# Kernel tuning notes

Measured on AMD Instinct MI355X. Metric: run time of the kernel, lower is better.

## Reference

```python
import jax, jax.numpy as jnp
import numpy as np

N, C, IMG, HEADS = 512, 3, 32, 4
F = C * IMG * IMG          # 3072 node feature dim
E = 4096                   # edges without self loops
EPS = 1e-5                 # BatchNorm eps
SLOPE = 0.2                # GATv2 LeakyReLU negative slope


def bn(x, g, b, m, v):
    # eval-mode BatchNorm2d over channel dim 1
    inv = g / jnp.sqrt(v + EPS)
    return x * inv[None, :, None, None] + (b - m * inv)[None, :, None, None]


def conv1x1(x, W, b):
    # W: [out_c, in_c]
    return jnp.einsum('bchw,oc->bohw', x, W) + b[None, :, None, None]


def setup_inputs():
    key = jax.random.key(0)
    ks = jax.random.split(key, 32)
    inp = {}
    inp['x'] = jax.random.normal(ks[0], (N, C, IMG, IMG), jnp.float32)
    src = jax.random.randint(ks[1], (E,), 0, N)
    off = jax.random.randint(ks[2], (E,), 1, N)
    inp['edge_index'] = jnp.stack([src, (src + off) % N]).astype(jnp.int32)  # no self loops

    def w(k, shape, fan_in):
        return jax.random.normal(k, shape, jnp.float32) / np.sqrt(fan_in)

    i = 3
    def nk():
        nonlocal i; i += 1; return ks[i - 1]
    # grapher fc1: Conv2d(C,C,1)+BN
    inp['fc1_W'] = w(nk(), (C, C), C); inp['fc1_b'] = jnp.zeros((C,), jnp.float32)
    inp['bn1_g'] = jnp.ones((C,), jnp.float32); inp['bn1_b'] = jnp.zeros((C,), jnp.float32)
    inp['bn1_m'] = 0.1 * jax.random.normal(nk(), (C,), jnp.float32)
    inp['bn1_v'] = jax.random.uniform(nk(), (C,), jnp.float32, 0.5, 1.5)
    # GATv2Conv(F, F, heads=HEADS): lin_l, lin_r [F, HEADS*F] with bias, att [HEADS, F], out bias
    inp['Wl'] = w(nk(), (F, HEADS * F), F); inp['bl'] = jnp.zeros((HEADS * F,), jnp.float32)
    inp['Wr'] = w(nk(), (F, HEADS * F), F); inp['br'] = jnp.zeros((HEADS * F,), jnp.float32)
    inp['att'] = w(nk(), (HEADS, F), F)
    inp['gat_b'] = jnp.zeros((HEADS * F,), jnp.float32)
    # grapher fc2: Conv2d(C*HEADS, C, 1)+BN
    inp['fc2_W'] = w(nk(), (C, C * HEADS), C * HEADS); inp['fc2_b'] = jnp.zeros((C,), jnp.float32)
    inp['bn2_g'] = jnp.ones((C,), jnp.float32); inp['bn2_b'] = jnp.zeros((C,), jnp.float32)
    inp['bn2_m'] = 0.1 * jax.random.normal(nk(), (C,), jnp.float32)
    inp['bn2_v'] = jax.random.uniform(nk(), (C,), jnp.float32, 0.5, 1.5)
    # FFN fc1 / fc2 (C->C 1x1 conv + BN)
    inp['ffn1_W'] = w(nk(), (C, C), C); inp['ffn1_b'] = jnp.zeros((C,), jnp.float32)
    inp['bnf1_g'] = jnp.ones((C,), jnp.float32); inp['bnf1_b'] = jnp.zeros((C,), jnp.float32)
    inp['bnf1_m'] = 0.1 * jax.random.normal(nk(), (C,), jnp.float32)
    inp['bnf1_v'] = jax.random.uniform(nk(), (C,), jnp.float32, 0.5, 1.5)
    inp['ffn2_W'] = w(nk(), (C, C), C); inp['ffn2_b'] = jnp.zeros((C,), jnp.float32)
    inp['bnf2_g'] = jnp.ones((C,), jnp.float32); inp['bnf2_b'] = jnp.zeros((C,), jnp.float32)
    inp['bnf2_m'] = 0.1 * jax.random.normal(nk(), (C,), jnp.float32)
    inp['bnf2_v'] = jax.random.uniform(nk(), (C,), jnp.float32, 0.5, 1.5)
    return inp


def reference(x, edge_index, fc1_W, fc1_b, bn1_g, bn1_b, bn1_m, bn1_v,
              Wl, bl, Wr, br, att, gat_b,
              fc2_W, fc2_b, bn2_g, bn2_b, bn2_m, bn2_v,
              ffn1_W, ffn1_b, bnf1_g, bnf1_b, bnf1_m, bnf1_v,
              ffn2_W, ffn2_b, bnf2_g, bnf2_b, bnf2_m, bnf2_v):
    shortcut = x
    h = bn(conv1x1(x, fc1_W, fc1_b), bn1_g, bn1_b, bn1_m, bn1_v)
    hf = h.reshape(N, F)
    xl = (hf @ Wl + bl).reshape(N, HEADS, F)  # source transform
    xr = (hf @ Wr + br).reshape(N, HEADS, F)  # target transform
    # add self loops (PyG GATv2Conv default)
    loops = jnp.arange(N, dtype=edge_index.dtype)
    src = jnp.concatenate([edge_index[0], loops])
    dst = jnp.concatenate([edge_index[1], loops])
    # GATv2 edge scores: a . LeakyReLU(xl_j + xr_i)
    e = jax.nn.leaky_relu(xl[src] + xr[dst], negative_slope=SLOPE)  # [E+N, HEADS, F]
    logits = jnp.einsum('ehf,hf->eh', e, att)
    mx = jax.ops.segment_max(logits, dst, num_segments=N)
    ex = jnp.exp(logits - jax.lax.stop_gradient(mx)[dst])
    denom = jax.ops.segment_sum(ex, dst, num_segments=N)
    alpha = ex / denom[dst]                                          # segment softmax over targets
    agg = jax.ops.segment_sum(xl[src] * alpha[:, :, None], dst, num_segments=N)  # [N, HEADS, F]
    g_out = (agg.reshape(N, HEADS * F) + gat_b).reshape(N, C * HEADS, IMG, IMG)
    g = bn(conv1x1(g_out, fc2_W, fc2_b), bn2_g, bn2_b, bn2_m, bn2_v) + shortcut
    # FFN with residual
    f = jax.nn.relu(bn(conv1x1(g, ffn1_W, ffn1_b), bnf1_g, bnf1_b, bnf1_m, bnf1_v))
    f = bn(conv1x1(f, ffn2_W, ffn2_b), bnf2_g, bnf2_b, bnf2_m, bnf2_v)
    return f + g
```

## Files before the change

### kernel.cpp

```cpp
#include <hip/hip_runtime.h>

#define N_NODES 512
#define FDIM    3072
#define HEADS   4
#define HFD     12288
#define E_IN    4096
#define E_TOT   4608
#define EPSV    1e-5f
#define SLOPE   0.2f
#define LCAP    256

typedef unsigned short u16;
typedef unsigned int   u32;

typedef short s16x8 __attribute__((ext_vector_type(8)));
typedef float f32x4 __attribute__((ext_vector_type(4)));

__device__ __forceinline__ u16 f2bf(float f){
  u32 u = __builtin_bit_cast(u32, f);
  u = (u + 0x7fffu + ((u >> 16) & 1u)) >> 16;
  return (u16)u;
}
__device__ __forceinline__ float bf2f(u16 h){
  return __builtin_bit_cast(float, ((u32)h) << 16);
}
__device__ __forceinline__ float bflo(u32 p){
  return __builtin_bit_cast(float, p << 16);
}
__device__ __forceinline__ float bfhi(u32 p){
  return __builtin_bit_cast(float, p & 0xffff0000u);
}

__device__ __forceinline__ void gl_lds16(const u16* g, u16* l){
  __builtin_amdgcn_global_load_lds(
      (const __attribute__((address_space(1))) unsigned int*)g,
      (__attribute__((address_space(3))) unsigned int*)l, 16, 0, 0);
}

__global__ void k_csr(const int* __restrict__ ei, int* __restrict__ cnt,
                      int* __restrict__ off, int* __restrict__ elist){
  __shared__ int s[512];
  __shared__ int cur[512];
  int t = threadIdx.x;
  s[t] = 0;
  __syncthreads();
  for (int e = t; e < E_TOT; e += 512){
    int d = (e < E_IN) ? ei[E_IN + e] : (e - E_IN);
    atomicAdd(&s[d], 1);
  }
  __syncthreads();
  int v = s[t];
  cnt[t] = v;
  for (int dd = 1; dd < 512; dd <<= 1){
    int add = (t >= dd) ? s[t - dd] : 0;
    __syncthreads();
    s[t] += add;
    __syncthreads();
  }
  int exc = s[t] - v;
  off[t] = exc;
  cur[t] = exc;
  __syncthreads();
  for (int e = t; e < E_TOT; e += 512){
    int d = (e < E_IN) ? ei[E_IN + e] : (e - E_IN);
    int pos = atomicAdd(&cur[d], 1);
    elist[pos] = e;
  }
}

__global__ void k_fc1(const float* __restrict__ x, const float* __restrict__ W,
                      const float* __restrict__ b, const float* __restrict__ g,
                      const float* __restrict__ bb, const float* __restrict__ m,
                      const float* __restrict__ v, u16* __restrict__ hf){
  int id = blockIdx.x * 256 + threadIdx.x;
  int n = id >> 10, p = id & 1023;
  float x0 = x[n * FDIM + p];
  float x1 = x[n * FDIM + 1024 + p];
  float x2 = x[n * FDIM + 2048 + p];
#pragma unroll
  for (int c = 0; c < 3; ++c){
    float t = b[c] + W[c*3+0]*x0 + W[c*3+1]*x1 + W[c*3+2]*x2;
    float inv = g[c] * rsqrtf(v[c] + EPSV);
    float o = t * inv + (bb[c] - m[c] * inv);
    hf[n * FDIM + c * 1024 + p] = f2bf(o);
  }
}

__global__ __launch_bounds__(256, 3) void k_gemm(
    const u16* __restrict__ hf, const float* __restrict__ Wl,
    const float* __restrict__ bl, const float* __restrict__ Wr,
    const float* __restrict__ br, u16* __restrict__ xl, u16* __restrict__ xr){
  __shared__ u16 As[2][256 * 32];
  __shared__ u16 Bs[2][64 * 40];

  const int tid  = threadIdx.x;
  const int wave = tid >> 6, lane = tid & 63;
  const int quad = lane >> 4, l16 = lane & 15;

  const int g = blockIdx.x;
  const int ntile = (g >> 4) * 8 + (g & 7);
  const int mhalf = (g >> 3) & 1;
  const int n0 = ntile * 64;
  const int rbase = mhalf * 256;

  const float* Wg; const float* biasp; u16* outp; int cb;
  if (n0 < HFD){ Wg = Wl; biasp = bl; outp = xl; cb = n0; }
  else         { Wg = Wr; biasp = br; outp = xr; cb = n0 - HFD; }

  const u16* ga = hf + (size_t)(rbase + wave * 64 + (lane >> 2)) * FDIM
                     + (((lane & 3) ^ ((lane >> 3) & 3)) << 3);

  const int bn = tid & 63, bkh = tid >> 6;
  const float* gb = Wg + (size_t)bkh * 8 * HFD + (cb + bn);
  const int bwo = bn * 40 + bkh * 8;

  const int araw = (wave * 64 + l16) * 32 + ((quad ^ ((l16 >> 1) & 3)) << 3);
  const int brd  = l16 * 40 + quad * 8;

  f32x4 acc[4][4];
#pragma unroll
  for (int i = 0; i < 4; ++i)
#pragma unroll
    for (int j = 0; j < 4; ++j) acc[i][j] = (f32x4){0.f, 0.f, 0.f, 0.f};

  float bv[8];
#pragma unroll
  for (int j = 0; j < 8; ++j) bv[j] = gb[(size_t)j * HFD];
#pragma unroll
  for (int i = 0; i < 4; ++i)
    gl_lds16(ga + (size_t)i * 16 * FDIM, As[0] + (wave * 4 + i) * 512);
  {
    u32 p0 = (u32)f2bf(bv[0]) | ((u32)f2bf(bv[1]) << 16);
    u32 p1 = (u32)f2bf(bv[2]) | ((u32)f2bf(bv[3]) << 16);
    u32 p2 = (u32)f2bf(bv[4]) | ((u32)f2bf(bv[5]) << 16);
    u32 p3 = (u32)f2bf(bv[6]) | ((u32)f2bf(bv[7]) << 16);
    *(uint4*)(Bs[0] + bwo) = make_uint4(p0, p1, p2, p3);
  }
#pragma unroll
  for (int j = 0; j < 8; ++j) bv[j] = gb[(size_t)(32 + j) * HFD];
  __syncthreads();

#define GEMM_BODY(KS, CUR, NXT)                                               \
  {                                                                           \
    const int ksv = (KS);                                                     \
    if (ksv < 95){                                                            \
      _Pragma("unroll")                                                       \
      for (int i = 0; i < 4; ++i)                                             \
        gl_lds16(ga + (size_t)i * 16 * FDIM + (ksv + 1) * 32,                 \
                 As[NXT] + (wave * 4 + i) * 512);                             \
      u32 p0 = (u32)f2bf(bv[0]) | ((u32)f2bf(bv[1]) << 16);                   \
      u32 p1 = (u32)f2bf(bv[2]) | ((u32)f2bf(bv[3]) << 16);                   \
      u32 p2 = (u32)f2bf(bv[4]) | ((u32)f2bf(bv[5]) << 16);                   \
      u32 p3 = (u32)f2bf(bv[6]) | ((u32)f2bf(bv[7]) << 16);                   \
      *(uint4*)(Bs[NXT] + bwo) = make_uint4(p0, p1, p2, p3);                  \
      int kn = (ksv + 2 < 96 ? ksv + 2 : 95) * 32;                            \
      _Pragma("unroll")                                                       \
      for (int j = 0; j < 8; ++j) bv[j] = gb[(size_t)(kn + j) * HFD];         \
    }                                                                         \
    s16x8 af[4], bfr[4];                                                      \
    _Pragma("unroll")                                                         \
    for (int i = 0; i < 4; ++i)                                               \
      af[i] = __builtin_bit_cast(s16x8, *(const uint4*)(As[CUR] + araw + i * 512)); \
    _Pragma("unroll")                                                         \
    for (int j = 0; j < 4; ++j)                                               \
      bfr[j] = __builtin_bit_cast(s16x8, *(const uint4*)(Bs[CUR] + brd + j * 640)); \
    _Pragma("unroll")                                                         \
    for (int i = 0; i < 4; ++i)                                               \
      _Pragma("unroll")                                                       \
      for (int j = 0; j < 4; ++j)                                             \
        acc[i][j] = __builtin_amdgcn_mfma_f32_16x16x32_bf16(af[i], bfr[j], acc[i][j], 0, 0, 0); \
    __syncthreads();                                                          \
  }

  for (int ks = 0; ks < 96; ks += 2){
    GEMM_BODY(ks, 0, 1);
    GEMM_BODY(ks + 1, 1, 0);
  }
#undef GEMM_BODY

  float bj[4];
#pragma unroll
  for (int j = 0; j < 4; ++j) bj[j] = biasp[cb + j * 16 + l16];
#pragma unroll
  for (int i = 0; i < 4; ++i){
    int mrow = rbase + wave * 64 + i * 16 + quad * 4;
#pragma unroll
    for (int r = 0; r < 4; ++r){
      u16* orow = outp + (size_t)(mrow + r) * HFD + cb + l16;
#pragma unroll
      for (int j = 0; j < 4; ++j)
        orow[j * 16] = f2bf(acc[i][j][r] + bj[j]);
    }
  }
}

__global__ __launch_bounds__(256) void k_lsm(
    const int* __restrict__ ei, const int* __restrict__ cnt,
    const int* __restrict__ off, const int* __restrict__ elist,
    const u16* __restrict__ xl, const u16* __restrict__ xr,
    const float* __restrict__ att, float* __restrict__ alpha){
  __shared__ float s_log[LCAP][5];
  __shared__ int   s_e[LCAP];
  const int n = blockIdx.x;
  const int t = threadIdx.x;
  const int h = t >> 6, lane = t & 63;
  const int deg = cnt[n], st = off[n];
  const int f0 = lane * 48;

  float xrf[48], av[48];
  {
    const u16* xrp = xr + (size_t)n * HFD + h * FDIM + f0;
    const float* ap = att + h * FDIM + f0;
#pragma unroll
    for (int k = 0; k < 6; ++k){
      uint4 a = *(const uint4*)(xrp + k * 8);
      xrf[k*8+0]=bflo(a.x); xrf[k*8+1]=bfhi(a.x);
      xrf[k*8+2]=bflo(a.y); xrf[k*8+3]=bfhi(a.y);
      xrf[k*8+4]=bflo(a.z); xrf[k*8+5]=bfhi(a.z);
      xrf[k*8+6]=bflo(a.w); xrf[k*8+7]=bfhi(a.w);
      float4 w0 = *(const float4*)(ap + k * 8);
      float4 w1 = *(const float4*)(ap + k * 8 + 4);
      av[k*8+0]=w0.x; av[k*8+1]=w0.y; av[k*8+2]=w0.z; av[k*8+3]=w0.w;
      av[k*8+4]=w1.x; av[k*8+5]=w1.y; av[k*8+6]=w1.z; av[k*8+7]=w1.w;
    }
  }

  auto edge_logit = [&](int s_node) -> float {
    const u16* xlp = xl + (size_t)s_node * HFD + h * FDIM + f0;
    float acc = 0.f;
#pragma unroll
    for (int k = 0; k < 6; ++k){
      uint4 a = *(const uint4*)(xlp + k * 8);
      float z;
      z = bflo(a.x) + xrf[k*8+0]; z = z > 0.f ? z : SLOPE * z; acc += z * av[k*8+0];
      z = bfhi(a.x) + xrf[k*8+1]; z = z > 0.f ? z : SLOPE * z; acc += z * av[k*8+1];
      z = bflo(a.y) + xrf[k*8+2]; z = z > 0.f ? z : SLOPE * z; acc += z * av[k*8+2];
      z = bfhi(a.y) + xrf[k*8+3]; z = z > 0.f ? z : SLOPE * z; acc += z * av[k*8+3];
      z = bflo(a.z) + xrf[k*8+4]; z = z > 0.f ? z : SLOPE * z; acc += z * av[k*8+4];
      z = bfhi(a.z) + xrf[k*8+5]; z = z > 0.f ? z : SLOPE * z; acc += z * av[k*8+5];
      z = bflo(a.w) + xrf[k*8+6]; z = z > 0.f ? z : SLOPE * z; acc += z * av[k*8+6];
      z = bfhi(a.w) + xrf[k*8+7]; z = z > 0.f ? z : SLOPE * z; acc += z * av[k*8+7];
    }
#pragma unroll
    for (int o = 32; o > 0; o >>= 1) acc += __shfl_down(acc, o);
    return acc;
  };

  if (deg <= LCAP){
    for (int jb = 0; jb < deg; ++jb){
      int e = elist[st + jb];
      if (t == 0) s_e[jb] = e;
      int s = (e < E_IN) ? ei[e] : (e - E_IN);
      float lg = edge_logit(s);
      if (lane == 0) s_log[jb][h] = lg;
    }
    __syncthreads();
    float mx = -1e30f;
    for (int j = lane; j < deg; j += 64) mx = fmaxf(mx, s_log[j][h]);
#pragma unroll
    for (int o = 32; o > 0; o >>= 1) mx = fmaxf(mx, __shfl_down(mx, o));
    mx = __shfl(mx, 0);
    float sm = 0.f;
    for (int j = lane; j < deg; j += 64) sm += __expf(s_log[j][h] - mx);
#pragma unroll
    for (int o = 32; o > 0; o >>= 1) sm += __shfl_down(sm, o);
    sm = __shfl(sm, 0);
    float rs = 1.f / sm;
    for (int j = lane; j < deg; j += 64)
      alpha[s_e[j] * 4 + h] = __expf(s_log[j][h] - mx) * rs;
  } else {
    for (int jb = 0; jb < deg; ++jb){
      int e = elist[st + jb];
      int s = (e < E_IN) ? ei[e] : (e - E_IN);
      float lg = edge_logit(s);
      if (lane == 0) alpha[e * 4 + h] = lg;
    }
    float mx = -1e30f;
    for (int j = lane; j < deg; j += 64){
      int e = elist[st + j];
      mx = fmaxf(mx, alpha[e * 4 + h]);
    }
#pragma unroll
    for (int o = 32; o > 0; o >>= 1) mx = fmaxf(mx, __shfl_down(mx, o));
    mx = __shfl(mx, 0);
    float sm = 0.f;
    for (int j = lane; j < deg; j += 64){
      int e = elist[st + j];
      sm += __expf(alpha[e * 4 + h] - mx);
    }
#pragma unroll
    for (int o = 32; o > 0; o >>= 1) sm += __shfl_down(sm, o);
    sm = __shfl(sm, 0);
    float rs = 1.f / sm;
    for (int j = lane; j < deg; j += 64){
      int e = elist[st + j];
      alpha[e * 4 + h] = __expf(alpha[e * 4 + h] - mx) * rs;
    }
  }
}

__global__ __launch_bounds__(256) void k_aggfinal(
    const int* __restrict__ ei, const int* __restrict__ cnt,
    const int* __restrict__ off, const int* __restrict__ elist,
    const float* __restrict__ alpha, const u16* __restrict__ xl,
    const float* __restrict__ gat_b,
    const float* __restrict__ W2, const float* __restrict__ b2,
    const float* __restrict__ g2, const float* __restrict__ bb2,
    const float* __restrict__ m2, const float* __restrict__ v2,
    const float* __restrict__ W3, const float* __restrict__ b3,
    const float* __restrict__ g3, const float* __restrict__ bb3,
    const float* __restrict__ m3, const float* __restrict__ v3,
    const float* __restrict__ W4, const float* __restrict__ b4,
    const float* __restrict__ g4, const float* __restrict__ bb4,
    const float* __restrict__ m4, const float* __restrict__ v4,
    const float* __restrict__ x, float* __restrict__ out){
  __shared__ int    s_src[128];
  __shared__ float4 s_al[128];
  const int n = blockIdx.x;
  const int t = threadIdx.x;
  const int p4 = t * 4;
  const int deg = cnt[n], st = off[n];

  float acc[12][4];
#pragma unroll
  for (int o = 0; o < 12; ++o)
#pragma unroll
    for (int r = 0; r < 4; ++r) acc[o][r] = 0.f;

  for (int base = 0; base < deg; base += 128){
    int cn = min(deg - base, 128);
    if (t < cn){
      int e = elist[st + base + t];
      s_src[t] = (e < E_IN) ? ei[e] : (e - E_IN);
      s_al[t] = *(const float4*)(alpha + e * 4);
    }
    __syncthreads();
    for (int j = 0; j < cn; ++j){
      int s = s_src[j];
      float4 al4 = s_al[j];
      float alh[4] = {al4.x, al4.y, al4.z, al4.w};
      const u16* bp = xl + (size_t)s * HFD;
#pragma unroll
      for (int h = 0; h < 4; ++h){
#pragma unroll
        for (int c = 0; c < 3; ++c){
          ushort4 xv = *(const ushort4*)(bp + h * FDIM + c * 1024 + p4);
          acc[h*3+c][0] += alh[h] * bf2f(xv.x);
          acc[h*3+c][1] += alh[h] * bf2f(xv.y);
          acc[h*3+c][2] += alh[h] * bf2f(xv.z);
          acc[h*3+c][3] += alh[h] * bf2f(xv.w);
        }
      }
    }
    __syncthreads();
  }

#pragma unroll
  for (int o = 0; o < 12; ++o){
    float4 gv = *(const float4*)(gat_b + o * 1024 + p4);
    acc[o][0] += gv.x; acc[o][1] += gv.y; acc[o][2] += gv.z; acc[o][3] += gv.w;
  }
  float xv[3][4];
#pragma unroll
  for (int c = 0; c < 3; ++c){
    float4 t4 = *(const float4*)(x + (size_t)n * FDIM + c * 1024 + p4);
    xv[c][0] = t4.x; xv[c][1] = t4.y; xv[c][2] = t4.z; xv[c][3] = t4.w;
  }
  float o4[3][4];
#pragma unroll
  for (int r = 0; r < 4; ++r){
    float gch[3];
#pragma unroll
    for (int c = 0; c < 3; ++c){
      float tt = b2[c];
#pragma unroll
      for (int o = 0; o < 12; ++o) tt += W2[c * 12 + o] * acc[o][r];
      float inv = g2[c] * rsqrtf(v2[c] + EPSV);
      gch[c] = tt * inv + (bb2[c] - m2[c] * inv) + xv[c][r];
    }
    float f1[3];
#pragma unroll
    for (int c = 0; c < 3; ++c){
      float tt = b3[c] + W3[c*3+0]*gch[0] + W3[c*3+1]*gch[1] + W3[c*3+2]*gch[2];
      float inv = g3[c] * rsqrtf(v3[c] + EPSV);
      float vv = tt * inv + (bb3[c] - m3[c] * inv);
      f1[c] = fmaxf(vv, 0.f);
    }
#pragma unroll
    for (int c = 0; c < 3; ++c){
      float tt = b4[c] + W4[c*3+0]*f1[0] + W4[c*3+1]*f1[1] + W4[c*3+2]*f1[2];
      float inv = g4[c] * rsqrtf(v4[c] + EPSV);
      o4[c][r] = tt * inv + (bb4[c] - m4[c] * inv) + gch[c];
    }
  }
#pragma unroll
  for (int c = 0; c < 3; ++c)
    *(float4*)(out + (size_t)n * FDIM + c * 1024 + p4) =
        make_float4(o4[c][0], o4[c][1], o4[c][2], o4[c][3]);
}

extern "C" void kernel_launch(void* const* d_in, const int* in_sizes, int n_in,
                              void* d_out, int out_size, void* d_ws, size_t ws_size,
                              hipStream_t stream){
  (void)in_sizes; (void)n_in; (void)out_size; (void)ws_size;
  const float* x     = (const float*)d_in[0];
  const int*   ei    = (const int*)d_in[1];
  const float* fc1_W = (const float*)d_in[2];
  const float* fc1_b = (const float*)d_in[3];
  const float* bn1_g = (const float*)d_in[4];
  const float* bn1_b = (const float*)d_in[5];
  const float* bn1_m = (const float*)d_in[6];
  const float* bn1_v = (const float*)d_in[7];
  const float* Wl    = (const float*)d_in[8];
  const float* bl    = (const float*)d_in[9];
  const float* Wr    = (const float*)d_in[10];
  const float* br    = (const float*)d_in[11];
  const float* att   = (const float*)d_in[12];
  const float* gat_b = (const float*)d_in[13];
  const float* fc2_W = (const float*)d_in[14];
  const float* fc2_b = (const float*)d_in[15];
  const float* bn2_g = (const float*)d_in[16];
  const float* bn2_b = (const float*)d_in[17];
  const float* bn2_m = (const float*)d_in[18];
  const float* bn2_v = (const float*)d_in[19];
  const float* ffn1_W= (const float*)d_in[20];
  const float* ffn1_b= (const float*)d_in[21];
  const float* bnf1_g= (const float*)d_in[22];
  const float* bnf1_b= (const float*)d_in[23];
  const float* bnf1_m= (const float*)d_in[24];
  const float* bnf1_v= (const float*)d_in[25];
  const float* ffn2_W= (const float*)d_in[26];
  const float* ffn2_b= (const float*)d_in[27];
  const float* bnf2_g= (const float*)d_in[28];
  const float* bnf2_b= (const float*)d_in[29];
  const float* bnf2_m= (const float*)d_in[30];
  const float* bnf2_v= (const float*)d_in[31];

  char* w = (char*)d_ws;
  u16*   hf     = (u16*)(w);
  u16*   xl     = (u16*)(w + 3145728);
  u16*   xr     = (u16*)(w + 15728640);
  float* alpha  = (float*)(w + 28385280);
  int*   cnt    = (int*)(w + 28459008);
  int*   offp   = (int*)(w + 28461056);
  int*   elist  = (int*)(w + 28465152);

  k_csr<<<1, 512, 0, stream>>>(ei, cnt, offp, elist);
  k_fc1<<<2048, 256, 0, stream>>>(x, fc1_W, fc1_b, bn1_g, bn1_b, bn1_m, bn1_v, hf);
  k_gemm<<<768, 256, 0, stream>>>(hf, Wl, bl, Wr, br, xl, xr);
  k_lsm<<<512, 256, 0, stream>>>(ei, cnt, offp, elist, xl, xr, att, alpha);
  k_aggfinal<<<512, 256, 0, stream>>>(ei, cnt, offp, elist, alpha, xl, gat_b,
                                      fc2_W, fc2_b, bn2_g, bn2_b, bn2_m, bn2_v,
                                      ffn1_W, ffn1_b, bnf1_g, bnf1_b, bnf1_m, bnf1_v,
                                      ffn2_W, ffn2_b, bnf2_g, bnf2_b, bnf2_m, bnf2_v,
                                      x, (float*)d_out);
}
```

Baseline: 525.1 us.

## Fuse CSR build into fc1 kernel and fuse softmax with aggregation

```diff
diff --git a/kernel.cpp b/kernel.cpp
--- a/kernel.cpp
+++ b/kernel.cpp
@@ -8,7 +8,7 @@
 #define E_TOT   4608
 #define EPSV    1e-5f
 #define SLOPE   0.2f
-#define LCAP    256
+#define LCAP    128
 
 typedef unsigned short u16;
 typedef unsigned int   u32;
@@ -37,52 +37,54 @@
       (__attribute__((address_space(3))) unsigned int*)l, 16, 0, 0);
 }
 
-__global__ void k_csr(const int* __restrict__ ei, int* __restrict__ cnt,
-                      int* __restrict__ off, int* __restrict__ elist){
-  __shared__ int s[512];
-  __shared__ int cur[512];
-  int t = threadIdx.x;
-  s[t] = 0;
-  __syncthreads();
-  for (int e = t; e < E_TOT; e += 512){
-    int d = (e < E_IN) ? ei[E_IN + e] : (e - E_IN);
-    atomicAdd(&s[d], 1);
-  }
-  __syncthreads();
-  int v = s[t];
-  cnt[t] = v;
-  for (int dd = 1; dd < 512; dd <<= 1){
-    int add = (t >= dd) ? s[t - dd] : 0;
-    __syncthreads();
-    s[t] += add;
-    __syncthreads();
-  }
-  int exc = s[t] - v;
-  off[t] = exc;
-  cur[t] = exc;
-  __syncthreads();
-  for (int e = t; e < E_TOT; e += 512){
-    int d = (e < E_IN) ? ei[E_IN + e] : (e - E_IN);
-    int pos = atomicAdd(&cur[d], 1);
-    elist[pos] = e;
-  }
-}
-
-__global__ void k_fc1(const float* __restrict__ x, const float* __restrict__ W,
-                      const float* __restrict__ b, const float* __restrict__ g,
-                      const float* __restrict__ bb, const float* __restrict__ m,
-                      const float* __restrict__ v, u16* __restrict__ hf){
-  int id = blockIdx.x * 256 + threadIdx.x;
-  int n = id >> 10, p = id & 1023;
-  float x0 = x[n * FDIM + p];
-  float x1 = x[n * FDIM + 1024 + p];
-  float x2 = x[n * FDIM + 2048 + p];
-#pragma unroll
-  for (int c = 0; c < 3; ++c){
-    float t = b[c] + W[c*3+0]*x0 + W[c*3+1]*x1 + W[c*3+2]*x2;
-    float inv = g[c] * rsqrtf(v[c] + EPSV);
-    float o = t * inv + (bb[c] - m[c] * inv);
-    hf[n * FDIM + c * 1024 + p] = f2bf(o);
+__global__ __launch_bounds__(256) void k_pre(
+    const float* __restrict__ x, const float* __restrict__ W,
+    const float* __restrict__ b, const float* __restrict__ g,
+    const float* __restrict__ bb, const float* __restrict__ m,
+    const float* __restrict__ v, u16* __restrict__ hf,
+    const int* __restrict__ ei, int* __restrict__ cnt,
+    int* __restrict__ off, int* __restrict__ elist){
+  if (blockIdx.x < 2048){
+    int id = blockIdx.x * 256 + threadIdx.x;
+    int n = id >> 10, p = id & 1023;
+    float x0 = x[n * FDIM + p];
+    float x1 = x[n * FDIM + 1024 + p];
+    float x2 = x[n * FDIM + 2048 + p];
+#pragma unroll
+    for (int c = 0; c < 3; ++c){
+      float t = b[c] + W[c*3+0]*x0 + W[c*3+1]*x1 + W[c*3+2]*x2;
+      float inv = g[c] * rsqrtf(v[c] + EPSV);
+      float o = t * inv + (bb[c] - m[c] * inv);
+      hf[n * FDIM + c * 1024 + p] = f2bf(o);
+    }
+  } else {
+    __shared__ int sa[512], sb[512];
+    int t = threadIdx.x;
+    sa[t] = 0; sa[t + 256] = 0;
+    __syncthreads();
+    for (int e = t; e < E_TOT; e += 256){
+      int d = (e < E_IN) ? ei[E_IN + e] : (e - E_IN);
+      atomicAdd(&sa[d], 1);
+    }
+    __syncthreads();
+    int c0 = sa[t], c1 = sa[t + 256];
+    cnt[t] = c0; cnt[t + 256] = c1;
+    int* src = sa; int* dst = sb;
+    for (int d = 1; d < 512; d <<= 1){
+      dst[t] = src[t] + (t >= d ? src[t - d] : 0);
+      int i2 = t + 256;
+      dst[i2] = src[i2] + (i2 >= d ? src[i2 - d] : 0);
+      __syncthreads();
+      int* tmp = src; src = dst; dst = tmp;
+    }
+    off[t] = src[t] - c0; off[t + 256] = src[t + 256] - c1;
+    dst[t] = src[t] - c0; dst[t + 256] = src[t + 256] - c1;
+    __syncthreads();
+    for (int e = t; e < E_TOT; e += 256){
+      int d = (e < E_IN) ? ei[E_IN + e] : (e - E_IN);
+      int pos = atomicAdd(&dst[d], 1);
+      elist[pos] = e;
+    }
   }
 }
 
@@ -194,13 +196,25 @@
   }
 }
 
-__global__ __launch_bounds__(256) void k_lsm(
+__global__ __launch_bounds__(256) void k_post(
     const int* __restrict__ ei, const int* __restrict__ cnt,
     const int* __restrict__ off, const int* __restrict__ elist,
     const u16* __restrict__ xl, const u16* __restrict__ xr,
-    const float* __restrict__ att, float* __restrict__ alpha){
+    const float* __restrict__ att, float* __restrict__ alpha,
+    const float* __restrict__ gat_b,
+    const float* __restrict__ W2, const float* __restrict__ b2,
+    const float* __restrict__ g2, const float* __restrict__ bb2,
+    const float* __restrict__ m2, const float* __restrict__ v2,
+    const float* __restrict__ W3, const float* __restrict__ b3,
+    const float* __restrict__ g3, const float* __restrict__ bb3,
+    const float* __restrict__ m3, const float* __restrict__ v3,
+    const float* __restrict__ W4, const float* __restrict__ b4,
+    const float* __restrict__ g4, const float* __restrict__ bb4,
+    const float* __restrict__ m4, const float* __restrict__ v4,
+    const float* __restrict__ x, float* __restrict__ out){
   __shared__ float s_log[LCAP][5];
-  __shared__ int   s_e[LCAP];
+  __shared__ __align__(16) float s_alf[LCAP][4];
+  __shared__ int s_src[LCAP];
   const int n = blockIdx.x;
   const int t = threadIdx.x;
   const int h = t >> 6, lane = t & 63;
@@ -246,11 +260,12 @@
     return acc;
   };
 
-  if (deg <= LCAP){
+  const bool small = (deg <= LCAP);
+  if (small){
     for (int jb = 0; jb < deg; ++jb){
       int e = elist[st + jb];
-      if (t == 0) s_e[jb] = e;
       int s = (e < E_IN) ? ei[e] : (e - E_IN);
+      if (t == 0) s_src[jb] = s;
       float lg = edge_logit(s);
       if (lane == 0) s_log[jb][h] = lg;
     }
@@ -267,7 +282,8 @@
     sm = __shfl(sm, 0);
     float rs = 1.f / sm;
     for (int j = lane; j < deg; j += 64)
-      alpha[s_e[j] * 4 + h] = __expf(s_log[j][h] - mx) * rs;
+      s_alf[j][h] = __expf(s_log[j][h] - mx) * rs;
+    __syncthreads();
   } else {
     for (int jb = 0; jb < deg; ++jb){
       int e = elist[st + jb];
@@ -275,6 +291,7 @@
       float lg = edge_logit(s);
       if (lane == 0) alpha[e * 4 + h] = lg;
     }
+    __syncthreads();
     float mx = -1e30f;
     for (int j = lane; j < deg; j += 64){
       int e = elist[st + j];
@@ -296,63 +313,60 @@
       int e = elist[st + j];
       alpha[e * 4 + h] = __expf(alpha[e * 4 + h] - mx) * rs;
     }
-  }
-}
-
-__global__ __launch_bounds__(256) void k_aggfinal(
-    const int* __restrict__ ei, const int* __restrict__ cnt,
-    const int* __restrict__ off, const int* __restrict__ elist,
-    const float* __restrict__ alpha, const u16* __restrict__ xl,
-    const float* __restrict__ gat_b,
-    const float* __restrict__ W2, const float* __restrict__ b2,
-    const float* __restrict__ g2, const float* __restrict__ bb2,
-    const float* __restrict__ m2, const float* __restrict__ v2,
-    const float* __restrict__ W3, const float* __restrict__ b3,
-    const float* __restrict__ g3, const float* __restrict__ bb3,
-    const float* __restrict__ m3, const float* __restrict__ v3,
-    const float* __restrict__ W4, const float* __restrict__ b4,
-    const float* __restrict__ g4, const float* __restrict__ bb4,
-    const float* __restrict__ m4, const float* __restrict__ v4,
-    const float* __restrict__ x, float* __restrict__ out){
-  __shared__ int    s_src[128];
-  __shared__ float4 s_al[128];
-  const int n = blockIdx.x;
-  const int t = threadIdx.x;
+    __syncthreads();
+  }
+
   const int p4 = t * 4;
-  const int deg = cnt[n], st = off[n];
-
   float acc[12][4];
 #pragma unroll
   for (int o = 0; o < 12; ++o)
 #pragma unroll
     for (int r = 0; r < 4; ++r) acc[o][r] = 0.f;
 
-  for (int base = 0; base < deg; base += 128){
-    int cn = min(deg - base, 128);
-    if (t < cn){
-      int e = elist[st + base + t];
-      s_src[t] = (e < E_IN) ? ei[e] : (e - E_IN);
-      s_al[t] = *(const float4*)(alpha + e * 4);
-    }
-    __syncthreads();
-    for (int j = 0; j < cn; ++j){
+  if (small){
+    for (int j = 0; j < deg; ++j){
       int s = s_src[j];
-      float4 al4 = s_al[j];
-      float alh[4] = {al4.x, al4.y, al4.z, al4.w};
+      float alh[4] = {s_alf[j][0], s_alf[j][1], s_alf[j][2], s_alf[j][3]};
       const u16* bp = xl + (size_t)s * HFD;
 #pragma unroll
-      for (int h = 0; h < 4; ++h){
+      for (int hh = 0; hh < 4; ++hh){
 #pragma unroll
         for (int c = 0; c < 3; ++c){
-          ushort4 xv = *(const ushort4*)(bp + h * FDIM + c * 1024 + p4);
-          acc[h*3+c][0] += alh[h] * bf2f(xv.x);
-          acc[h*3+c][1] += alh[h] * bf2f(xv.y);
-          acc[h*3+c][2] += alh[h] * bf2f(xv.z);
-          acc[h*3+c][3] += alh[h] * bf2f(xv.w);
+          ushort4 xv = *(const ushort4*)(bp + hh * FDIM + c * 1024 + p4);
+          acc[hh*3+c][0] += alh[hh] * bf2f(xv.x);
+          acc[hh*3+c][1] += alh[hh] * bf2f(xv.y);
+          acc[hh*3+c][2] += alh[hh] * bf2f(xv.z);
+          acc[hh*3+c][3] += alh[hh] * bf2f(xv.w);
         }
       }
     }
-    __syncthreads();
+  } else {
+    for (int base = 0; base < deg; base += LCAP){
+      int cn = min(deg - base, LCAP);
+      if (t < cn){
+        int e = elist[st + base + t];
+        s_src[t] = (e < E_IN) ? ei[e] : (e - E_IN);
+        *(float4*)&s_alf[t][0] = *(const float4*)(alpha + e * 4);
+      }
+      __syncthreads();
+      for (int j = 0; j < cn; ++j){
+        int s = s_src[j];
+        float alh[4] = {s_alf[j][0], s_alf[j][1], s_alf[j][2], s_alf[j][3]};
+        const u16* bp = xl + (size_t)s * HFD;
+#pragma unroll
+        for (int hh = 0; hh < 4; ++hh){
+#pragma unroll
+          for (int c = 0; c < 3; ++c){
+            ushort4 xv = *(const ushort4*)(bp + hh * FDIM + c * 1024 + p4);
+            acc[hh*3+c][0] += alh[hh] * bf2f(xv.x);
+            acc[hh*3+c][1] += alh[hh] * bf2f(xv.y);
+            acc[hh*3+c][2] += alh[hh] * bf2f(xv.z);
+            acc[hh*3+c][3] += alh[hh] * bf2f(xv.w);
+          }
+        }
+      }
+      __syncthreads();
+    }
   }
 
 #pragma unroll
@@ -445,13 +459,13 @@
   int*   offp   = (int*)(w + 28461056);
   int*   elist  = (int*)(w + 28465152);
 
-  k_csr<<<1, 512, 0, stream>>>(ei, cnt, offp, elist);
-  k_fc1<<<2048, 256, 0, stream>>>(x, fc1_W, fc1_b, bn1_g, bn1_b, bn1_m, bn1_v, hf);
+  k_pre<<<2049, 256, 0, stream>>>(x, fc1_W, fc1_b, bn1_g, bn1_b, bn1_m, bn1_v,
+                                  hf, ei, cnt, offp, elist);
   k_gemm<<<768, 256, 0, stream>>>(hf, Wl, bl, Wr, br, xl, xr);
-  k_lsm<<<512, 256, 0, stream>>>(ei, cnt, offp, elist, xl, xr, att, alpha);
-  k_aggfinal<<<512, 256, 0, stream>>>(ei, cnt, offp, elist, alpha, xl, gat_b,
-                                      fc2_W, fc2_b, bn2_g, bn2_b, bn2_m, bn2_v,
-                                      ffn1_W, ffn1_b, bnf1_g, bnf1_b, bnf1_m, bnf1_v,
-                                      ffn2_W, ffn2_b, bnf2_g, bnf2_b, bnf2_m, bnf2_v,
-                                      x, (float*)d_out);
-}
+  k_post<<<512, 256, 0, stream>>>(ei, cnt, offp, elist, xl, xr, att, alpha,
+                                  gat_b,
+                                  fc2_W, fc2_b, bn2_g, bn2_b, bn2_m, bn2_v,
+                                  ffn1_W, ffn1_b, bnf1_g, bnf1_b, bnf1_m, bnf1_v,
+                                  ffn2_W, ffn2_b, bnf2_g, bnf2_b, bnf2_m, bnf2_v,
+                                  x, (float*)d_out);
+}
```

After: 523.9 us. About the same (-0.2%).
